# Kernel tuning notes

Measured on AMD Instinct MI355X. Metric: run time of the kernel, lower is better.

Reference implementation:

```python
import jax, jax.numpy as jnp
import numpy as np

B, S, D = 2, 2048, 2048
QC, KVC = 16, 4          # query heads, kv heads (GQA)
HD = D // QC             # head_dim = 128
FF = 8192                # ff_dim = 4 * model_dim
EPS = 1e-5


def rotate_every_two(x):
    x1 = x[..., ::2]
    x2 = x[..., 1::2]
    return jnp.stack((-x2, x1), axis=-1).reshape(*x.shape[:-1], -1)


def apply_rope(x, seq_len, sin, cos):
    sin = sin[:seq_len]
    cos = cos[:seq_len]
    return x * cos + rotate_every_two(x) * sin


def rmsnorm(x, w, eps=EPS):
    xf = x.astype(jnp.float32)
    xf = xf * jax.lax.rsqrt(jnp.square(xf).mean(-1, keepdims=True) + eps)
    return xf.astype(x.dtype) * w


def attention(x, mask, sin, cos, wqkv, wo):
    b, s, d = x.shape
    kv_repeat = QC // KVC
    qkv = x @ wqkv
    q = qkv[..., :D].reshape(b, s, kv_repeat, KVC, HD)
    q = jnp.moveaxis(q, 1, 3)                       # (b, rep, kvc, s, hd)
    q = apply_rope(q, s, sin, cos)
    k, v = jnp.split(qkv[..., D:], 2, axis=-1)
    k = k.reshape(b, s, KVC, HD).swapaxes(1, 2)     # (b, kvc, s, hd)
    v = v.reshape(b, s, KVC, HD).swapaxes(1, 2)
    k = apply_rope(k, s, sin, cos) * (HD ** -0.5)
    k = k[:, None]                                  # (b, 1, kvc, s, hd)
    v = v[:, None]
    a = q @ k.swapaxes(-2, -1)                      # (b, rep, kvc, s, s)
    a = a + mask[:s, :s]
    a = jax.nn.softmax(a, axis=-1)
    o = a @ v                                       # (b, rep, kvc, s, hd)
    o = o.reshape(b, QC, s, HD).swapaxes(1, 2).reshape(b, s, d)
    return o @ wo


def ffn(x, wk, wv):
    k = jnp.square(jax.nn.relu(x @ wk))
    return k @ wv


def setup_inputs() -> dict:
    key = jax.random.key(0)
    ks = jax.random.split(key, 6)
    std = 0.02
    x = jax.random.normal(ks[0], (B, S, D), jnp.float32)
    wqkv = std * jax.random.normal(ks[1], (D, D + 2 * KVC * HD), jnp.float32)
    wo = std * jax.random.normal(ks[2], (D, D), jnp.float32)
    ffn_wk = std * jax.random.normal(ks[3], (D, FF), jnp.float32)
    ffn_wv = std * jax.random.normal(ks[4], (FF, D), jnp.float32)
    norm1_w = jnp.ones((D,), jnp.float32)
    norm2_w = jnp.ones((D,), jnp.float32)
    # GPT-J style interleaved RoPE tables of shape (S, HD)
    pos = jnp.arange(S, dtype=jnp.float32)
    inv_freq = 1.0 / (10000.0 ** (jnp.arange(0, HD, 2, dtype=jnp.float32) / HD))
    freqs = pos[:, None] * inv_freq[None, :]
    rope_sin = jnp.repeat(jnp.sin(freqs), 2, axis=-1)
    rope_cos = jnp.repeat(jnp.cos(freqs), 2, axis=-1)
    # additive causal mask
    mask = jnp.where(jnp.tril(jnp.ones((S, S), bool)), 0.0, -1e9).astype(jnp.float32)
    return dict(x=x, mask=mask, rope_sin=rope_sin, rope_cos=rope_cos,
                wqkv=wqkv, wo=wo, norm1_w=norm1_w, norm2_w=norm2_w,
                ffn_wk=ffn_wk, ffn_wv=ffn_wv)


def reference(x, mask, rope_sin, rope_cos, wqkv, wo, norm1_w, norm2_w, ffn_wk, ffn_wv):
    # pre-norm residual block
    x = x + attention(rmsnorm(x, norm1_w), mask, rope_sin, rope_cos, wqkv, wo)
    x = x + ffn(rmsnorm(x, norm2_w), ffn_wk, ffn_wv)
    return x
```

## Files before the change

### kernel.cpp

```cpp
#include <hip/hip_runtime.h>
#include <hip/hip_bf16.h>
#include <cstdint>
#include <cstddef>
#include <type_traits>

typedef __hip_bfloat16 bf16;
typedef float f32x4 __attribute__((ext_vector_type(4)));
typedef short s16x8 __attribute__((ext_vector_type(8)));

#define BB 2
#define SS 2048
#define DD 2048
#define QCH 16
#define KVH 4
#define HD 128
#define FF 8192

__device__ __forceinline__ float b2f(bf16 v) { return __bfloat162float(v); }
__device__ __forceinline__ bf16 f2b(float v) { return __float2bfloat16(v); }

__device__ __forceinline__ void gl_lds16(const void* g, void* l) {
    __builtin_amdgcn_global_load_lds((const __attribute__((address_space(1))) void*)g,
                                     (__attribute__((address_space(3))) void*)l,
                                     16, 0, 0);
}

__global__ __launch_bounds__(256) void transpose_cast(const float* __restrict__ src,
                                                      bf16* __restrict__ dst,
                                                      int K, int N) {
    __shared__ float t[32][33];
    int n0 = blockIdx.x * 32, k0 = blockIdx.y * 32;
    int tx = threadIdx.x, ty = threadIdx.y;
#pragma unroll
    for (int j = 0; j < 4; ++j)
        t[ty + j * 8][tx] = src[(size_t)(k0 + ty + j * 8) * N + n0 + tx];
    __syncthreads();
#pragma unroll
    for (int j = 0; j < 4; ++j)
        dst[(size_t)(n0 + ty + j * 8) * K + k0 + tx] = f2b(t[tx][ty + j * 8]);
}

__global__ __launch_bounds__(256) void rmsnorm_k(const float* __restrict__ x,
                                                 const float* __restrict__ w,
                                                 bf16* __restrict__ out) {
    int row = blockIdx.x;
    int tid = threadIdx.x;
    const float* xr = x + (size_t)row * DD + tid * 8;
    f32x4 a0 = *(const f32x4*)xr;
    f32x4 a1 = *(const f32x4*)(xr + 4);
    float f[8];
    float ss = 0.f;
#pragma unroll
    for (int i = 0; i < 4; ++i) { f[i] = a0[i]; f[i + 4] = a1[i]; }
#pragma unroll
    for (int i = 0; i < 8; ++i) ss += f[i] * f[i];
#pragma unroll
    for (int off = 32; off > 0; off >>= 1) ss += __shfl_down(ss, off);
    __shared__ float red[4];
    int lane = tid & 63, wv_ = tid >> 6;
    if (lane == 0) red[wv_] = ss;
    __syncthreads();
    float tot = red[0] + red[1] + red[2] + red[3];
    float scale = rsqrtf(tot * (1.0f / DD) + 1e-5f);
#pragma unroll
    for (int i = 0; i < 8; ++i) {
        int col = tid * 8 + i;
        out[(size_t)row * DD + col] = f2b(f[i] * scale * w[col]);
    }
}

__global__ __launch_bounds__(256) void rope_scatter(const bf16* __restrict__ qkv,
                                                    const float* __restrict__ rsin,
                                                    const float* __restrict__ rcos,
                                                    bf16* __restrict__ q_r,
                                                    bf16* __restrict__ k_r,
                                                    bf16* __restrict__ v_t) {
    int p = blockIdx.x * 256 + threadIdx.x;
    int row = p / 1536;
    int c2 = p - row * 1536;
    int col = c2 * 2;
    int b = row >> 11, s = row & 2047;
    size_t qbase = (size_t)row * 3072 + col;
    float e = b2f(qkv[qbase]);
    float o = b2f(qkv[qbase + 1]);
    if (col < 2048) {
        int h = col >> 7, hd = col & 127;
        float cs = rcos[s * HD + hd];
        float sn = rsin[s * HD + hd];
        size_t base = (((size_t)(b * QCH + h)) * SS + s) * HD + hd;
        q_r[base]     = f2b(e * cs - o * sn);
        q_r[base + 1] = f2b(o * cs + e * sn);
    } else if (col < 2560) {
        int cc = col - 2048;
        int kc = cc >> 7, hd = cc & 127;
        float cs = rcos[s * HD + hd];
        float sn = rsin[s * HD + hd];
        const float kscale = 0.08838834764831845f;
        size_t base = (((size_t)(b * KVH + kc)) * SS + s) * HD + hd;
        k_r[base]     = f2b((e * cs - o * sn) * kscale);
        k_r[base + 1] = f2b((o * cs + e * sn) * kscale);
    } else {
        int cc = col - 2560;
        int kc = cc >> 7, hd = cc & 127;
        size_t base = (((size_t)(b * KVH + kc)) * HD + hd) * SS + s;
        v_t[base]      = qkv[qbase];
        v_t[base + SS] = qkv[qbase + 1];
    }
}

template <int EPI, typename CT>
__global__ __launch_bounds__(256) void gemm_bt(const bf16* __restrict__ A,
                                               const bf16* __restrict__ Bt,
                                               const float* __restrict__ res,
                                               CT* __restrict__ C,
                                               int M, int N, int K) {
    __shared__ __align__(16) bf16 As[2][128 * 32];
    __shared__ __align__(16) bf16 Bs[2][128 * 32];
    const int tid = threadIdx.x;
    const int m0 = blockIdx.y * 128, n0 = blockIdx.x * 128;
    const int lane = tid & 63, w = tid >> 6;
    const int wm = (w >> 1) * 64, wn = (w & 1) * 64;
    const int lm = lane & 15, quad = lane >> 4;

    const int fo = tid * 16;
    const int row0 = tid >> 2;
    const int cb0 = (((tid & 3) ^ ((tid >> 3) & 3)) * 16);

    const char* Ab0 = (const char*)A + (size_t)(m0 + row0) * K * 2 + cb0;
    const char* Ab1 = (const char*)A + (size_t)(m0 + row0 + 64) * K * 2 + cb0;
    const char* Bb0 = (const char*)Bt + (size_t)(n0 + row0) * K * 2 + cb0;
    const char* Bb1 = (const char*)Bt + (size_t)(n0 + row0 + 64) * K * 2 + cb0;

    f32x4 acc[4][4];
    const f32x4 zero = {0.f, 0.f, 0.f, 0.f};
#pragma unroll
    for (int i = 0; i < 4; ++i)
#pragma unroll
        for (int j = 0; j < 4; ++j) acc[i][j] = zero;

    const int NT = K >> 5;
    {
        gl_lds16(Ab0, (char*)&As[0][0] + fo);
        gl_lds16(Ab1, (char*)&As[0][0] + fo + 4096);
        gl_lds16(Bb0, (char*)&Bs[0][0] + fo);
        gl_lds16(Bb1, (char*)&Bs[0][0] + fo + 4096);
    }
    const int sw = (quad ^ ((lm >> 1) & 3)) * 8;

    for (int kt = 0; kt < NT; ++kt) {
        const int cur = kt & 1;
        __syncthreads();
        if (kt + 1 < NT) {
            const int kb = (kt + 1) * 64;
            gl_lds16(Ab0 + kb, (char*)&As[cur ^ 1][0] + fo);
            gl_lds16(Ab1 + kb, (char*)&As[cur ^ 1][0] + fo + 4096);
            gl_lds16(Bb0 + kb, (char*)&Bs[cur ^ 1][0] + fo);
            gl_lds16(Bb1 + kb, (char*)&Bs[cur ^ 1][0] + fo + 4096);
        }
        s16x8 af[4], bfr[4];
#pragma unroll
        for (int mi = 0; mi < 4; ++mi)
            af[mi] = *(const s16x8*)&As[cur][(wm + mi * 16 + lm) * 32 + sw];
#pragma unroll
        for (int ni = 0; ni < 4; ++ni)
            bfr[ni] = *(const s16x8*)&Bs[cur][(wn + ni * 16 + lm) * 32 + sw];
#pragma unroll
        for (int mi = 0; mi < 4; ++mi)
#pragma unroll
            for (int ni = 0; ni < 4; ++ni)
                acc[mi][ni] = __builtin_amdgcn_mfma_f32_16x16x32_bf16(af[mi], bfr[ni], acc[mi][ni], 0, 0, 0);
    }

#pragma unroll
    for (int mi = 0; mi < 4; ++mi)
#pragma unroll
        for (int ni = 0; ni < 4; ++ni) {
            int gr = m0 + wm + mi * 16 + quad * 4;
            int gc = n0 + wn + ni * 16 + lm;
#pragma unroll
            for (int r = 0; r < 4; ++r) {
                size_t idx = (size_t)(gr + r) * N + gc;
                float v = acc[mi][ni][r];
                if (EPI == 1) v += res[idx];
                if (EPI == 2) { v = fmaxf(v, 0.f); v = v * v; }
                if constexpr (std::is_same<CT, float>::value) C[idx] = v;
                else C[idx] = f2b(v);
            }
        }
}

__global__ __launch_bounds__(256) void attn_k(const bf16* __restrict__ q_r,
                                              const bf16* __restrict__ k_r,
                                              const bf16* __restrict__ v_t,
                                              bf16* __restrict__ o_buf) {
    __shared__ __align__(16) bf16 Ps[4][32 * 72];
    const int qt = blockIdx.x, h = blockIdx.y, b = blockIdx.z;
    const int tid = threadIdx.x, w = tid >> 6, lane = tid & 63;
    const int lm = lane & 15, quad = lane >> 4;
    const int kvh = h & (KVH - 1);
    const int qw0 = qt * 128 + w * 32;
    bf16* Pw = &Ps[w][0];

    s16x8 aq[2][4];
#pragma unroll
    for (int mt = 0; mt < 2; ++mt) {
        const bf16* qp = q_r + (((size_t)(b * QCH + h)) * SS + qw0 + mt * 16 + lm) * HD + quad * 8;
#pragma unroll
        for (int c = 0; c < 4; ++c) aq[mt][c] = *(const s16x8*)(qp + c * 32);
    }

    const bf16* kbase = k_r + ((size_t)(b * KVH + kvh)) * SS * HD;
    const bf16* vbase = v_t + ((size_t)(b * KVH + kvh)) * HD * SS;

    const f32x4 zero = {0.f, 0.f, 0.f, 0.f};
    f32x4 accO[2][8];
#pragma unroll
    for (int mt = 0; mt < 2; ++mt)
#pragma unroll
        for (int ni = 0; ni < 8; ++ni) accO[mt][ni] = zero;
    float lp[2][4] = {{0.f, 0.f, 0.f, 0.f}, {0.f, 0.f, 0.f, 0.f}};

    const int ntiles = (qw0 + 95) >> 6;
    for (int kt = 0; kt < ntiles; ++kt) {
        const int kb = kt * 64;
#pragma unroll
        for (int nt = 0; nt < 4; ++nt) {
            const bf16* kp = kbase + (size_t)(kb + nt * 16 + lm) * HD + quad * 8;
            s16x8 kf[4];
#pragma unroll
            for (int c = 0; c < 4; ++c) kf[c] = *(const s16x8*)(kp + c * 32);
            const int colk = kb + nt * 16 + lm;
#pragma unroll
            for (int mt = 0; mt < 2; ++mt) {
                f32x4 sc = zero;
#pragma unroll
                for (int c = 0; c < 4; ++c)
                    sc = __builtin_amdgcn_mfma_f32_16x16x32_bf16(aq[mt][c], kf[c], sc, 0, 0, 0);
#pragma unroll
                for (int r = 0; r < 4; ++r) {
                    int rowq = qw0 + mt * 16 + quad * 4 + r;
                    float p = (colk <= rowq) ? __expf(sc[r]) : 0.f;
                    lp[mt][r] += p;
                    Pw[(mt * 16 + quad * 4 + r) * 72 + nt * 16 + lm] = f2b(p);
                }
            }
        }
        s16x8 pf[2][2];
#pragma unroll
        for (int mt = 0; mt < 2; ++mt)
#pragma unroll
            for (int kf2 = 0; kf2 < 2; ++kf2)
                pf[mt][kf2] = *(const s16x8*)&Pw[(mt * 16 + lm) * 72 + kf2 * 32 + quad * 8];
#pragma unroll
        for (int ni = 0; ni < 8; ++ni) {
            const bf16* vp = vbase + (size_t)(ni * 16 + lm) * SS + kb + quad * 8;
#pragma unroll
            for (int kf2 = 0; kf2 < 2; ++kf2) {
                s16x8 vf = *(const s16x8*)(vp + kf2 * 32);
#pragma unroll
                for (int mt = 0; mt < 2; ++mt)
                    accO[mt][ni] = __builtin_amdgcn_mfma_f32_16x16x32_bf16(pf[mt][kf2], vf, accO[mt][ni], 0, 0, 0);
            }
        }
    }

#pragma unroll
    for (int mt = 0; mt < 2; ++mt)
#pragma unroll
        for (int r = 0; r < 4; ++r) {
            float l = lp[mt][r];
#pragma unroll
            for (int off = 1; off < 16; off <<= 1) l += __shfl_xor(l, off);
            lp[mt][r] = 1.f / l;
        }

#pragma unroll
    for (int mt = 0; mt < 2; ++mt)
#pragma unroll
        for (int ni = 0; ni < 8; ++ni)
#pragma unroll
            for (int r = 0; r < 4; ++r) {
                int s = qw0 + mt * 16 + quad * 4 + r;
                size_t idx = ((size_t)(b * SS + s)) * DD + h * HD + ni * 16 + lm;
                o_buf[idx] = f2b(accO[mt][ni][r] * lp[mt][r]);
            }
}

extern "C" void kernel_launch(void* const* d_in, const int* in_sizes, int n_in,
                              void* d_out, int out_size, void* d_ws, size_t ws_size,
                              hipStream_t stream) {
    const float* x    = (const float*)d_in[0];
    const float* rsin = (const float*)d_in[2];
    const float* rcos = (const float*)d_in[3];
    const float* wqkv = (const float*)d_in[4];
    const float* wo   = (const float*)d_in[5];
    const float* n1w  = (const float*)d_in[6];
    const float* n2w  = (const float*)d_in[7];
    const float* wk   = (const float*)d_in[8];
    const float* wv   = (const float*)d_in[9];
    float* out = (float*)d_out;

    char* ws = (char*)d_ws;
    size_t off = 0;
    auto allocb = [&](size_t elems) { bf16* p = (bf16*)(ws + off); off += elems * 2; return p; };
    auto allocf = [&](size_t elems) { float* p = (float*)(ws + off); off += elems * 4; return p; };
    bf16* wqkvT = allocb((size_t)3072 * 2048);
    bf16* woT   = allocb((size_t)2048 * 2048);
    bf16* wkT   = allocb((size_t)8192 * 2048);
    bf16* wvT   = allocb((size_t)2048 * 8192);
    bf16* xn    = allocb((size_t)4096 * 2048);
    bf16* qkv   = allocb((size_t)4096 * 3072);
    bf16* q_r   = allocb((size_t)BB * QCH * SS * HD);
    bf16* k_r   = allocb((size_t)BB * KVH * SS * HD);
    bf16* v_t   = allocb((size_t)BB * KVH * HD * SS);
    bf16* ffnh  = allocb((size_t)4096 * 8192);
    float* x1   = allocf((size_t)4096 * 2048);

    dim3 tb(32, 8);
    transpose_cast<<<dim3(3072 / 32, 2048 / 32), tb, 0, stream>>>(wqkv, wqkvT, 2048, 3072);
    transpose_cast<<<dim3(2048 / 32, 2048 / 32), tb, 0, stream>>>(wo, woT, 2048, 2048);
    transpose_cast<<<dim3(8192 / 32, 2048 / 32), tb, 0, stream>>>(wk, wkT, 2048, 8192);
    transpose_cast<<<dim3(2048 / 32, 8192 / 32), tb, 0, stream>>>(wv, wvT, 8192, 2048);

    rmsnorm_k<<<4096, 256, 0, stream>>>(x, n1w, xn);
    gemm_bt<0, bf16><<<dim3(3072 / 128, 4096 / 128), 256, 0, stream>>>(xn, wqkvT, nullptr, qkv, 4096, 3072, 2048);
    rope_scatter<<<(4096 * 1536) / 256, 256, 0, stream>>>(qkv, rsin, rcos, q_r, k_r, v_t);
    attn_k<<<dim3(SS / 128, QCH, BB), 256, 0, stream>>>(q_r, k_r, v_t, qkv );
    gemm_bt<1, float><<<dim3(2048 / 128, 4096 / 128), 256, 0, stream>>>(qkv, woT, x, x1, 4096, 2048, 2048);
    rmsnorm_k<<<4096, 256, 0, stream>>>(x1, n2w, xn);
    gemm_bt<2, bf16><<<dim3(8192 / 128, 4096 / 128), 256, 0, stream>>>(xn, wkT, nullptr, ffnh, 4096, 8192, 2048);
    gemm_bt<1, float><<<dim3(2048 / 128, 4096 / 128), 256, 0, stream>>>(ffnh, wvT, x1, out, 4096, 2048, 8192);
}
```

Before: 993.5 us.

## Stage K/V tiles in swizzled LDS shared across waves in attention kernel

The attention kernel now loads each 64-key K tile and its matching V tile once per block into XOR-swizzled shared memory using global-to-LDS loads. The four waves then read their MFMA fragments from LDS instead of each fetching the same K/V from global memory. This cuts redundant global traffic but adds two block barriers per tile. Because the tile count is now uniform across the block, waves with no causal work idle while the others compute. The grid is also flattened to 1D with the query-tile index in the high bits, which changes the order blocks are scheduled.

```diff
diff --git a/kernel.cpp b/kernel.cpp
--- a/kernel.cpp
+++ b/kernel.cpp
@@ -193,8 +193,12 @@
                                               const bf16* __restrict__ k_r,
                                               const bf16* __restrict__ v_t,
                                               bf16* __restrict__ o_buf) {
+    __shared__ __align__(16) bf16 Ks[64 * 128];
+    __shared__ __align__(16) bf16 Vs[128 * 64];
     __shared__ __align__(16) bf16 Ps[4][32 * 72];
-    const int qt = blockIdx.x, h = blockIdx.y, b = blockIdx.z;
+    const int i = blockIdx.x;
+    const int qt = i >> 5, hb = i & 31;
+    const int h = hb & 15, b = hb >> 4;
     const int tid = threadIdx.x, w = tid >> 6, lane = tid & 63;
     const int lm = lane & 15, quad = lane >> 4;
     const int kvh = h & (KVH - 1);
@@ -209,8 +213,12 @@
         for (int c = 0; c < 4; ++c) aq[mt][c] = *(const s16x8*)(qp + c * 32);
     }
 
-    const bf16* kbase = k_r + ((size_t)(b * KVH + kvh)) * SS * HD;
-    const bf16* vbase = v_t + ((size_t)(b * KVH + kvh)) * HD * SS;
+    const char* kbase = (const char*)(k_r + ((size_t)(b * KVH + kvh)) * SS * HD);
+    const char* vbase = (const char*)(v_t + ((size_t)(b * KVH + kvh)) * HD * SS);
+
+    const int krow = tid >> 4, kslot = tid & 15;
+    const int ksrc_off = ((kslot ^ (krow & 15)) * 16);
+    const int vrow = tid >> 3, vslot = tid & 7;
 
     const f32x4 zero = {0.f, 0.f, 0.f, 0.f};
     f32x4 accO[2][8];
@@ -220,48 +228,66 @@
         for (int ni = 0; ni < 8; ++ni) accO[mt][ni] = zero;
     float lp[2][4] = {{0.f, 0.f, 0.f, 0.f}, {0.f, 0.f, 0.f, 0.f}};
 
-    const int ntiles = (qw0 + 95) >> 6;
+    const int ntiles = 2 * qt + 2;
     for (int kt = 0; kt < ntiles; ++kt) {
         const int kb = kt * 64;
 #pragma unroll
-        for (int nt = 0; nt < 4; ++nt) {
-            const bf16* kp = kbase + (size_t)(kb + nt * 16 + lm) * HD + quad * 8;
-            s16x8 kf[4];
-#pragma unroll
-            for (int c = 0; c < 4; ++c) kf[c] = *(const s16x8*)(kp + c * 32);
-            const int colk = kb + nt * 16 + lm;
-#pragma unroll
-            for (int mt = 0; mt < 2; ++mt) {
-                f32x4 sc = zero;
+        for (int j = 0; j < 4; ++j) {
+            int kr = krow + j * 16;
+            gl_lds16(kbase + (size_t)(kb + kr) * 256 + ksrc_off, (char*)Ks + tid * 16 + j * 4096);
+        }
+#pragma unroll
+        for (int j = 0; j < 4; ++j) {
+            int vr = vrow + j * 32;
+            gl_lds16(vbase + (size_t)vr * (SS * 2) + kb * 2 + ((vslot ^ (vr & 7)) * 16),
+                     (char*)Vs + tid * 16 + j * 4096);
+        }
+        __syncthreads();
+
+        const bool active = (kb <= qw0 + 31);
+        if (active) {
+#pragma unroll
+            for (int nt = 0; nt < 4; ++nt) {
+                const int krl = nt * 16 + lm;
+                s16x8 kf[4];
 #pragma unroll
                 for (int c = 0; c < 4; ++c)
-                    sc = __builtin_amdgcn_mfma_f32_16x16x32_bf16(aq[mt][c], kf[c], sc, 0, 0, 0);
-#pragma unroll
-                for (int r = 0; r < 4; ++r) {
-                    int rowq = qw0 + mt * 16 + quad * 4 + r;
-                    float p = (colk <= rowq) ? __expf(sc[r]) : 0.f;
-                    lp[mt][r] += p;
-                    Pw[(mt * 16 + quad * 4 + r) * 72 + nt * 16 + lm] = f2b(p);
+                    kf[c] = *(const s16x8*)((char*)Ks + krl * 256 + (((c * 4 + quad) ^ lm) * 16));
+                const int colk = kb + krl;
+#pragma unroll
+                for (int mt = 0; mt < 2; ++mt) {
+                    f32x4 sc = zero;
+#pragma unroll
+                    for (int c = 0; c < 4; ++c)
+                        sc = __builtin_amdgcn_mfma_f32_16x16x32_bf16(aq[mt][c], kf[c], sc, 0, 0, 0);
+#pragma unroll
+                    for (int r = 0; r < 4; ++r) {
+                        int rowq = qw0 + mt * 16 + quad * 4 + r;
+                        float p = (colk <= rowq) ? __expf(sc[r]) : 0.f;
+                        lp[mt][r] += p;
+                        Pw[(mt * 16 + quad * 4 + r) * 72 + nt * 16 + lm] = f2b(p);
+                    }
                 }
             }
-        }
-        s16x8 pf[2][2];
-#pragma unroll
-        for (int mt = 0; mt < 2; ++mt)
-#pragma unroll
-            for (int kf2 = 0; kf2 < 2; ++kf2)
-                pf[mt][kf2] = *(const s16x8*)&Pw[(mt * 16 + lm) * 72 + kf2 * 32 + quad * 8];
-#pragma unroll
-        for (int ni = 0; ni < 8; ++ni) {
-            const bf16* vp = vbase + (size_t)(ni * 16 + lm) * SS + kb + quad * 8;
-#pragma unroll
-            for (int kf2 = 0; kf2 < 2; ++kf2) {
-                s16x8 vf = *(const s16x8*)(vp + kf2 * 32);
-#pragma unroll
-                for (int mt = 0; mt < 2; ++mt)
-                    accO[mt][ni] = __builtin_amdgcn_mfma_f32_16x16x32_bf16(pf[mt][kf2], vf, accO[mt][ni], 0, 0, 0);
+            s16x8 pf[2][2];
+#pragma unroll
+            for (int mt = 0; mt < 2; ++mt)
+#pragma unroll
+                for (int kf2 = 0; kf2 < 2; ++kf2)
+                    pf[mt][kf2] = *(const s16x8*)&Pw[(mt * 16 + lm) * 72 + kf2 * 32 + quad * 8];
+#pragma unroll
+            for (int ni = 0; ni < 8; ++ni) {
+                const int vrl = ni * 16 + lm;
+#pragma unroll
+                for (int kf2 = 0; kf2 < 2; ++kf2) {
+                    s16x8 vf = *(const s16x8*)((char*)Vs + vrl * 128 + (((kf2 * 4 + quad) ^ (lm & 7)) * 16));
+#pragma unroll
+                    for (int mt = 0; mt < 2; ++mt)
+                        accO[mt][ni] = __builtin_amdgcn_mfma_f32_16x16x32_bf16(pf[mt][kf2], vf, accO[mt][ni], 0, 0, 0);
+                }
             }
         }
+        __syncthreads();
     }
 
 #pragma unroll
@@ -325,7 +351,7 @@
     rmsnorm_k<<<4096, 256, 0, stream>>>(x, n1w, xn);
     gemm_bt<0, bf16><<<dim3(3072 / 128, 4096 / 128), 256, 0, stream>>>(xn, wqkvT, nullptr, qkv, 4096, 3072, 2048);
     rope_scatter<<<(4096 * 1536) / 256, 256, 0, stream>>>(qkv, rsin, rcos, q_r, k_r, v_t);
-    attn_k<<<dim3(SS / 128, QCH, BB), 256, 0, stream>>>(q_r, k_r, v_t, qkv );
+    attn_k<<<512, 256, 0, stream>>>(q_r, k_r, v_t, qkv );
     gemm_bt<1, float><<<dim3(2048 / 128, 4096 / 128), 256, 0, stream>>>(qkv, woT, x, x1, 4096, 2048, 2048);
     rmsnorm_k<<<4096, 256, 0, stream>>>(x1, n2w, xn);
     gemm_bt<2, bf16><<<dim3(8192 / 128, 4096 / 128), 256, 0, stream>>>(xn, wkT, nullptr, ffnh, 4096, 8192, 2048);
```

Result: faster. 865.5 us (-12.9%).
